# Kernel tuning notes

Hardware: AMD Instinct MI355X
Metric: run time of the kernel (lower is better)

The kernel has to match this reference:

```python
import jax, jax.numpy as jnp
import numpy as np

EMB = 256
N_NODES = 20000
N_EDGES = 200000


def _sage_layer(x, src, dst, edge_attr, W, b, n_nodes):
    # message = x[src] + edge_attr ; mean-aggregate into dst ; ReLU(Linear([x;agg]))
    msg = x[src] + edge_attr                                   # [2E, emb]
    s = jax.ops.segment_sum(msg, dst, num_segments=n_nodes)    # [N, emb]
    cnt = jax.ops.segment_sum(jnp.ones((dst.shape[0], 1), x.dtype), dst,
                              num_segments=n_nodes)            # [N, 1]
    agg = s / jnp.maximum(cnt, 1.0)
    return jax.nn.relu(jnp.concatenate([x, agg], axis=1) @ W + b)


def setup_inputs() -> dict:
    key = jax.random.key(0)
    ks = jax.random.split(key, 12)
    sc = 0.05
    inp = {
        "x": jax.random.normal(ks[0], (N_NODES, EMB), jnp.float32),
        "edge_attr": jax.random.normal(ks[1], (N_EDGES, EMB), jnp.float32),
        "batch_q_embds": jax.random.normal(ks[2], (N_EDGES, EMB), jnp.float32),
        "edge_index": jax.random.randint(ks[3], (2, N_EDGES), 0, N_NODES, jnp.int64
                                         if jax.config.jax_enable_x64 else jnp.int32),
        "W_rev1": jax.random.normal(ks[4], (EMB, EMB), jnp.float32) * sc,
        "b_rev1": jnp.zeros((EMB,), jnp.float32),
        "W_rev2": jax.random.normal(ks[5], (EMB, EMB), jnp.float32) * sc,
        "b_rev2": jnp.zeros((EMB,), jnp.float32),
        "W_sage1": jax.random.normal(ks[6], (2 * EMB, EMB), jnp.float32) * sc,
        "b_sage1": jnp.zeros((EMB,), jnp.float32),
        "W_sage2": jax.random.normal(ks[7], (2 * EMB, EMB), jnp.float32) * sc,
        "b_sage2": jnp.zeros((EMB,), jnp.float32),
        "W_pred1": jax.random.normal(ks[8], (6 * EMB, EMB), jnp.float32) * sc,
        "b_pred1": jnp.zeros((EMB,), jnp.float32),
        "W_pred2": jax.random.normal(ks[9], (EMB, 1), jnp.float32) * sc,
        "b_pred2": jnp.zeros((1,), jnp.float32),
    }
    return inp


def reference(x, edge_attr, batch_q_embds, edge_index,
              W_rev1, b_rev1, W_rev2, b_rev2,
              W_sage1, b_sage1, W_sage2, b_sage2,
              W_pred1, b_pred1, W_pred2, b_pred2):
    src, dst = edge_index[0], edge_index[1]
    # reverse-edge attributes via proj_reverse MLP
    edge_attr_rev = jax.nn.relu(edge_attr @ W_rev1 + b_rev1) @ W_rev2 + b_rev2
    src_f = jnp.concatenate([src, dst])          # [2E]
    dst_f = jnp.concatenate([dst, src])          # [2E]
    ea_f = jnp.concatenate([edge_attr, edge_attr_rev], axis=0)  # [2E, emb]
    # 2-layer GraphSAGE backbone over nodes, collect per-layer outputs
    h1 = _sage_layer(x, src_f, dst_f, ea_f, W_sage1, b_sage1, N_NODES)
    h2 = _sage_layer(h1, src_f, dst_f, ea_f, W_sage2, b_sage2, N_NODES)
    h_e = jnp.concatenate([h1, h2], axis=1)      # [N, 2*emb]
    # per-edge triple features: [q ; h_e[head] ; edge_attr ; h_e[tail]]
    h_triple = jnp.concatenate([batch_q_embds, h_e[src], edge_attr, h_e[dst]], axis=1)
    attn_logits = (jax.nn.relu(h_triple @ W_pred1 + b_pred1) @ W_pred2 + b_pred2)[:, 0]
    # idp-bern sampling (training=True): gumbel-like logistic noise, temp=1
    u = jax.random.uniform(jax.random.key(42), attn_logits.shape,
                           attn_logits.dtype, 1e-10, 1.0 - 1e-10)
    noise = jnp.log(u) - jnp.log(1.0 - u)
    sampled = jax.nn.sigmoid(attn_logits + noise)
    return attn_logits, sampled
```

## Files before the change

kernel.cpp:

```cpp
#include <hip/hip_runtime.h>
#include <cstdint>
#include <cstddef>

#define EMB 256
#define NN 20000
#define NE 200000
#define NE2 400000

typedef unsigned short ushort_t;
typedef __attribute__((ext_vector_type(8))) short bf16x8;
typedef __attribute__((ext_vector_type(4))) float f32x4;

__device__ __forceinline__ ushort_t f2bf(float f) {
    unsigned u = __float_as_uint(f);
    u += 0x7FFFu + ((u >> 16) & 1u);
    return (ushort_t)(u >> 16);
}
__device__ __forceinline__ float bf2f(ushort_t u) {
    return __uint_as_float(((unsigned)u) << 16);
}

__device__ __forceinline__ void async_cp16(const ushort_t* g, ushort_t* l) {
    __builtin_amdgcn_global_load_lds(
        (const __attribute__((address_space(1))) unsigned int*)g,
        (__attribute__((address_space(3))) unsigned int*)l,
        16, 0, 0);
}

__device__ __forceinline__ void pc_map(int bid, int T, int& p, int& colblk) {
    int Tf = T & ~15;
    if (bid < Tf) {
        p = (bid >> 4) * 8 + (bid & 7);
        colblk = (bid >> 3) & 1;
    } else {
        int rem = bid - Tf;
        int nr = (T - Tf) >> 1;
        p = (T >> 1) - nr + rem % nr;
        colblk = rem / nr;
    }
}

__device__ __forceinline__ unsigned rotl32(unsigned v, int d) {
    return (v << d) | (v >> (32 - d));
}
__device__ __forceinline__ void threefry2x32(unsigned k0, unsigned k1,
                                             unsigned x0, unsigned x1,
                                             unsigned& o0, unsigned& o1) {
    unsigned k2 = k0 ^ k1 ^ 0x1BD11BDAu;
    x0 += k0; x1 += k1;
#define TF_R(r) { x0 += x1; x1 = rotl32(x1, (r)); x1 ^= x0; }
    TF_R(13) TF_R(15) TF_R(26) TF_R(6)
    x0 += k1; x1 += k2 + 1u;
    TF_R(17) TF_R(29) TF_R(16) TF_R(24)
    x0 += k2; x1 += k0 + 2u;
    TF_R(13) TF_R(15) TF_R(26) TF_R(6)
    x0 += k0; x1 += k1 + 3u;
    TF_R(17) TF_R(29) TF_R(16) TF_R(24)
    x0 += k1; x1 += k2 + 4u;
    TF_R(13) TF_R(15) TF_R(26) TF_R(6)
    x0 += k2; x1 += k0 + 5u;
#undef TF_R
    o0 = x0; o1 = x1;
}

__global__ void deg_kernel(const int* __restrict__ src, const int* __restrict__ dst,
                           int* __restrict__ deg) {
    int i = blockIdx.x * blockDim.x + threadIdx.x;
    if (i < NE2) {
        int n = (i < NE) ? dst[i] : src[i - NE];
        atomicAdd(&deg[n], 1);
    }
}

__global__ void prefix_kernel(const int* __restrict__ deg, int* __restrict__ row_start,
                              int* __restrict__ cursor) {
    __shared__ int sums[1024];
    int t = threadIdx.x;
    const int CH = (NN + 1023) / 1024;
    int lo = t * CH, hi = lo + CH;
    if (hi > NN) hi = NN;
    if (lo > NN) lo = NN;
    int s = 0;
    for (int n = lo; n < hi; n++) s += deg[n];
    sums[t] = s;
    __syncthreads();
    for (int off = 1; off < 1024; off <<= 1) {
        int v = (t >= off) ? sums[t - off] : 0;
        __syncthreads();
        sums[t] += v;
        __syncthreads();
    }
    int run = (t == 0) ? 0 : sums[t - 1];
    for (int n = lo; n < hi; n++) {
        row_start[n] = run;
        cursor[n] = run;
        run += deg[n];
    }
    if (t == 1023) row_start[NN] = sums[1023];
}

__global__ void scatter_kernel(const int* __restrict__ src, const int* __restrict__ dst,
                               int* __restrict__ cursor, int* __restrict__ elist) {
    int i = blockIdx.x * blockDim.x + threadIdx.x;
    if (i < NE2) {
        int n = (i < NE) ? dst[i] : src[i - NE];
        int pos = atomicAdd(&cursor[n], 1);
        elist[pos] = i;
    }
}

__global__ void conv2_kernel(const float* __restrict__ a, ushort_t* __restrict__ oa, int na8,
                             const float* __restrict__ b, ushort_t* __restrict__ ob, int nb8) {
    int i = blockIdx.x * 256 + threadIdx.x;
    const float* p;
    ushort_t* o;
    if (i < na8) { p = a + (size_t)i * 8; o = oa + (size_t)i * 8; }
    else {
        int j = i - na8;
        if (j >= nb8) return;
        p = b + (size_t)j * 8; o = ob + (size_t)j * 8;
    }
    float4 u = *(const float4*)p;
    float4 v = *(const float4*)(p + 4);
    union { ushort_t s[8]; uint4 w; } r;
    r.s[0] = f2bf(u.x); r.s[1] = f2bf(u.y); r.s[2] = f2bf(u.z); r.s[3] = f2bf(u.w);
    r.s[4] = f2bf(v.x); r.s[5] = f2bf(v.y); r.s[6] = f2bf(v.z); r.s[7] = f2bf(v.w);
    *(uint4*)o = r.w;
}

struct TD { const float* src; ushort_t* dst; int stride, koff, kr; };
struct TA { TD d[8]; };

__global__ void transpose_all_kernel(TA ta) {
    TD t = ta.d[blockIdx.y];
    int k = blockIdx.x;
    if (k >= t.kr) return;
    int n = threadIdx.x;
    t.dst[(size_t)n * t.stride + t.koff + k] = f2bf(t.src[(size_t)k * 256 + n]);
}

__global__ __launch_bounds__(256, 3) void rev_fused_kernel(
        const ushort_t* __restrict__ ea_bf,
        const ushort_t* __restrict__ Wt1, const float* __restrict__ b1,
        const ushort_t* __restrict__ Wt2, const float* __restrict__ b2,
        ushort_t* __restrict__ ea_rev) {
    __shared__ ushort_t As[64 * 32];
    __shared__ ushort_t Bs[256 * 32];
    __shared__ ushort_t Hl[64 * 264];

    int tid = threadIdx.x;
    int lane = tid & 63, wave = tid >> 6;
    int wr = wave >> 1, wc = wave & 1;
    int quad = lane >> 4, col_l = lane & 15;
    int p = blockIdx.x;

    f32x4 acc[2][8];
#pragma unroll
    for (int mt = 0; mt < 2; mt++)
#pragma unroll
        for (int nt = 0; nt < 8; nt++) acc[mt][nt] = (f32x4)0.f;

    for (int k0 = 0; k0 < 256; k0 += 32) {
        __syncthreads();
        {
            int row = tid >> 2, ch = tid & 3;
            async_cp16(ea_bf + (size_t)(p * 64 + row) * 256 + k0 + ch * 8,
                       As + (wave * 64) * 8);
        }
#pragma unroll
        for (int j = 0; j < 4; j++) {
            int flat = tid + 256 * j;
            int n = flat >> 2, ch = flat & 3;
            async_cp16(Wt1 + (size_t)n * 256 + k0 + ch * 8,
                       Bs + (wave * 64 + 256 * j) * 8);
        }
        __syncthreads();
        bf16x8 a[2], b[8];
#pragma unroll
        for (int mt = 0; mt < 2; mt++)
            a[mt] = *(const bf16x8*)(As + (wr * 32 + mt * 16 + col_l) * 32 + quad * 8);
#pragma unroll
        for (int nt = 0; nt < 8; nt++)
            b[nt] = *(const bf16x8*)(Bs + (wc * 128 + nt * 16 + col_l) * 32 + quad * 8);
#pragma unroll
        for (int mt = 0; mt < 2; mt++)
#pragma unroll
            for (int nt = 0; nt < 8; nt++)
                acc[mt][nt] = __builtin_amdgcn_mfma_f32_16x16x32_bf16(
                    a[mt], b[nt], acc[mt][nt], 0, 0, 0);
    }

    __syncthreads();
#pragma unroll
    for (int nt = 0; nt < 8; nt++) {
        int lcol = wc * 128 + nt * 16 + col_l;
        float bb = b1[lcol];
#pragma unroll
        for (int mt = 0; mt < 2; mt++)
#pragma unroll
            for (int r = 0; r < 4; r++) {
                int lrow = wr * 32 + mt * 16 + quad * 4 + r;
                Hl[lrow * 264 + lcol] = f2bf(fmaxf(acc[mt][nt][r] + bb, 0.f));
            }
    }
#pragma unroll
    for (int mt = 0; mt < 2; mt++)
#pragma unroll
        for (int nt = 0; nt < 8; nt++) acc[mt][nt] = (f32x4)0.f;

    for (int k0 = 0; k0 < 256; k0 += 32) {
        __syncthreads();
#pragma unroll
        for (int j = 0; j < 4; j++) {
            int flat = tid + 256 * j;
            int n = flat >> 2, ch = flat & 3;
            async_cp16(Wt2 + (size_t)n * 256 + k0 + ch * 8,
                       Bs + (wave * 64 + 256 * j) * 8);
        }
        __syncthreads();
        bf16x8 a[2], b[8];
#pragma unroll
        for (int mt = 0; mt < 2; mt++)
            a[mt] = *(const bf16x8*)(Hl + (wr * 32 + mt * 16 + col_l) * 264
                                     + k0 + quad * 8);
#pragma unroll
        for (int nt = 0; nt < 8; nt++)
            b[nt] = *(const bf16x8*)(Bs + (wc * 128 + nt * 16 + col_l) * 32 + quad * 8);
#pragma unroll
        for (int mt = 0; mt < 2; mt++)
#pragma unroll
            for (int nt = 0; nt < 8; nt++)
                acc[mt][nt] = __builtin_amdgcn_mfma_f32_16x16x32_bf16(
                    a[mt], b[nt], acc[mt][nt], 0, 0, 0);
    }

#pragma unroll
    for (int nt = 0; nt < 8; nt++) {
        int colg = wc * 128 + nt * 16 + col_l;
        float bb = b2[colg];
#pragma unroll
        for (int mt = 0; mt < 2; mt++)
#pragma unroll
            for (int r = 0; r < 4; r++) {
                int rg = p * 64 + wr * 32 + mt * 16 + quad * 4 + r;
                ea_rev[(size_t)rg * 256 + colg] = f2bf(acc[mt][nt][r] + bb);
            }
    }
}

template <int KTOT, int EPI, bool A0F32>
__global__ __launch_bounds__(256, 4) void mfma_gemm(
        const void* __restrict__ A0v, int rsA0,
        const ushort_t* __restrict__ A1, int rsA1,
        const ushort_t* __restrict__ Bt, const ushort_t* __restrict__ Bt2,
        const float* __restrict__ bias,
        void* __restrict__ out, void* __restrict__ out2, int rsOut, int M,
        const int* __restrict__ srcp, const int* __restrict__ dstp,
        const float* __restrict__ Hs, const float* __restrict__ Hd,
        const float* __restrict__ w2) {
    __shared__ ushort_t As[2][128 * 32];
    __shared__ ushort_t Bs[2][128 * 32];
    __shared__ float red[128];

    int tid = threadIdx.x;
    int lane = tid & 63;
    int wave = tid >> 6;
    int wr = wave >> 1;
    int wc = wave & 1;
    int quad = lane >> 4;
    int col_l = lane & 15;
    int p, colblk;
    pc_map(blockIdx.x, gridDim.x, p, colblk);

    const ushort_t* Bsel = blockIdx.y ? Bt2 : Bt;
    void* Osel = blockIdx.y ? out2 : out;

    f32x4 acc[4][4];
#pragma unroll
    for (int mt = 0; mt < 4; mt++)
#pragma unroll
        for (int nt = 0; nt < 4; nt++) acc[mt][nt] = (f32x4)0.f;

    for (int k0 = 0; k0 < KTOT; k0 += 64) {
        __syncthreads();
#pragma unroll
        for (int h = 0; h < 2; h++) {
            int kk = k0 + 32 * h;
#pragma unroll
            for (int j = 0; j < 2; j++) {
                int flat = tid + 256 * j;
                int n = flat >> 2, ch = flat & 3;
                const ushort_t* gp = Bsel + (size_t)(colblk * 128 + n) * KTOT + kk + ch * 8;
                async_cp16(gp, Bs[h] + ((wave * 64 + 256 * j) * 8));
            }
            bool seg1 = (KTOT == 512) && (kk >= 256);
            if (A0F32 && !seg1) {
#pragma unroll
                for (int j = 0; j < 2; j++) {
                    int flat = tid + 256 * j;
                    int row = flat >> 2, ch = flat & 3;
                    int grow = p * 128 + row;
                    if (grow >= M) grow = M - 1;
                    const float* gp = (const float*)A0v + (size_t)grow * rsA0 + kk + ch * 8;
                    float4 u = *(const float4*)gp;
                    float4 v = *(const float4*)(gp + 4);
                    union { ushort_t s[8]; uint4 w; } r;
                    r.s[0] = f2bf(u.x); r.s[1] = f2bf(u.y); r.s[2] = f2bf(u.z); r.s[3] = f2bf(u.w);
                    r.s[4] = f2bf(v.x); r.s[5] = f2bf(v.y); r.s[6] = f2bf(v.z); r.s[7] = f2bf(v.w);
                    *(uint4*)(As[h] + (size_t)flat * 8) = r.w;
                }
            } else {
                const ushort_t* abase;
                int rs, koffs;
                if (KTOT == 512 && kk >= 256) { abase = A1; rs = rsA1; koffs = kk - 256; }
                else { abase = (const ushort_t*)A0v; rs = rsA0; koffs = kk; }
#pragma unroll
                for (int j = 0; j < 2; j++) {
                    int flat = tid + 256 * j;
                    int row = flat >> 2, ch = flat & 3;
                    int grow = p * 128 + row;
                    if (grow >= M) grow = M - 1;
                    const ushort_t* gp = abase + (size_t)grow * rs + koffs + ch * 8;
                    async_cp16(gp, As[h] + ((wave * 64 + 256 * j) * 8));
                }
            }
        }
        __syncthreads();

#pragma unroll
        for (int h = 0; h < 2; h++) {
            bf16x8 a[4], b[4];
#pragma unroll
            for (int mt = 0; mt < 4; mt++)
                a[mt] = *(const bf16x8*)(As[h] + (wr * 64 + mt * 16 + col_l) * 32 + quad * 8);
#pragma unroll
            for (int nt = 0; nt < 4; nt++)
                b[nt] = *(const bf16x8*)(Bs[h] + (wc * 64 + nt * 16 + col_l) * 32 + quad * 8);
#pragma unroll
            for (int mt = 0; mt < 4; mt++)
#pragma unroll
                for (int nt = 0; nt < 4; nt++)
                    acc[mt][nt] = __builtin_amdgcn_mfma_f32_16x16x32_bf16(
                        a[mt], b[nt], acc[mt][nt], 0, 0, 0);
        }
    }

    if (EPI == 4) {
        __syncthreads();
        if (tid < 128) red[tid] = 0.f;
        __syncthreads();
        float b1c[4], w2c[4];
#pragma unroll
        for (int nt = 0; nt < 4; nt++) {
            int col = colblk * 128 + wc * 64 + nt * 16 + col_l;
            b1c[nt] = bias[col];
            w2c[nt] = w2[col];
        }
#pragma unroll
        for (int mt = 0; mt < 4; mt++) {
#pragma unroll
            for (int r = 0; r < 4; r++) {
                int lrow = wr * 64 + mt * 16 + quad * 4 + r;
                int e = p * 128 + lrow;
                int ec = e < M ? e : M - 1;
                int s = srcp[ec], d = dstp[ec];
                const float* hsr = Hs + (size_t)s * 256;
                const float* hdr = Hd + (size_t)d * 256;
                float part = 0.f;
#pragma unroll
                for (int nt = 0; nt < 4; nt++) {
                    int col = colblk * 128 + wc * 64 + nt * 16 + col_l;
                    part += fmaxf(acc[mt][nt][r] + hsr[col] + hdr[col] + b1c[nt], 0.f)
                            * w2c[nt];
                }
#pragma unroll
                for (int m = 8; m > 0; m >>= 1) part += __shfl_xor(part, m, 64);
                if (col_l == 0) atomicAdd(&red[lrow], part);
            }
        }
        __syncthreads();
        if (tid < 128) {
            int e = p * 128 + tid;
            if (e < M) {
                float* tgt = colblk ? (float*)out2 : (float*)out;
                tgt[e] = red[tid];
            }
        }
        return;
    }

    float bs[4];
    if (EPI >= 2) {
#pragma unroll
        for (int nt = 0; nt < 4; nt++)
            bs[nt] = bias[colblk * 128 + wc * 64 + nt * 16 + col_l];
    }
#pragma unroll
    for (int mt = 0; mt < 4; mt++) {
#pragma unroll
        for (int nt = 0; nt < 4; nt++) {
            int colg = colblk * 128 + wc * 64 + nt * 16 + col_l;
#pragma unroll
            for (int r = 0; r < 4; r++) {
                int rg = p * 128 + wr * 64 + mt * 16 + quad * 4 + r;
                if (rg < M) {
                    float v = acc[mt][nt][r];
                    if (EPI >= 2) v += bs[nt];
                    if (EPI == 3) v = fmaxf(v, 0.f);
                    if (EPI == 0)
                        ((float*)Osel)[(size_t)rg * rsOut + colg] = v;
                    else
                        ((ushort_t*)Osel)[(size_t)rg * rsOut + colg] = f2bf(v);
                }
            }
        }
    }
}

__global__ void finalize_kernel(float* __restrict__ out, const float* __restrict__ part1,
                                const float* __restrict__ b2v, float* __restrict__ out_s) {
    int e = blockIdx.x * blockDim.x + threadIdx.x;
    if (e >= NE) return;
    float logit = out[e] + part1[e] + b2v[0];
    out[e] = logit;
    unsigned y0, y1;
    threefry2x32(0u, 42u, 0u, (unsigned)e, y0, y1);
    unsigned bits = y0 ^ y1;
    float f = __uint_as_float((bits >> 9) | 0x3F800000u) - 1.0f;
    float u = fmaxf(1e-10f, f + 1e-10f);
    float noise = logf(u) - logf(1.0f - u);
    out_s[e] = 1.0f / (1.0f + expf(-(logit + noise)));
}

__global__ __launch_bounds__(64) void agg_ea_kernel(
        const ushort_t* __restrict__ eaf, const ushort_t* __restrict__ ear,
        const int* __restrict__ row_start, const int* __restrict__ elist,
        float* __restrict__ agg_ea) {
    int n = blockIdx.x;
    int c = threadIdx.x * 4;
    float ax = 0.f, ay = 0.f, az = 0.f, aw = 0.f;
    int beg = row_start[n], end = row_start[n + 1];
    for (int p = beg; p < end; p++) {
        int i = elist[p];
        const ushort_t* er = (i < NE) ? eaf + (size_t)i * 256
                                      : ear + (size_t)(i - NE) * 256;
        ushort4 ev = *(const ushort4*)(er + c);
        ax += bf2f(ev.x); ay += bf2f(ev.y); az += bf2f(ev.z); aw += bf2f(ev.w);
    }
    float4 o; o.x = ax; o.y = ay; o.z = az; o.w = aw;
    *(float4*)(agg_ea + (size_t)n * 256 + c) = o;
}

__global__ __launch_bounds__(64) void agg_x_kernel(
        const ushort_t* __restrict__ xin, int rsx,
        const int* __restrict__ src, const int* __restrict__ dst,
        const int* __restrict__ row_start, const int* __restrict__ elist,
        const int* __restrict__ deg, const float* __restrict__ agg_ea,
        ushort_t* __restrict__ agg) {
    int n = blockIdx.x;
    int c = threadIdx.x * 4;
    float ax = 0.f, ay = 0.f, az = 0.f, aw = 0.f;
    int beg = row_start[n], end = row_start[n + 1];
    for (int p = beg; p < end; p++) {
        int i = elist[p];
        int node = (i < NE) ? src[i] : dst[i - NE];
        ushort4 xv = *(const ushort4*)(xin + (size_t)node * rsx + c);
        ax += bf2f(xv.x); ay += bf2f(xv.y); az += bf2f(xv.z); aw += bf2f(xv.w);
    }
    float4 e = *(const float4*)(agg_ea + (size_t)n * 256 + c);
    float d = fmaxf((float)deg[n], 1.0f);
    ushort4 o;
    o.x = f2bf((ax + e.x) / d); o.y = f2bf((ay + e.y) / d);
    o.z = f2bf((az + e.z) / d); o.w = f2bf((aw + e.w) / d);
    *(ushort4*)(agg + (size_t)n * 256 + c) = o;
}

extern "C" void kernel_launch(void* const* d_in, const int* in_sizes, int n_in,
                              void* d_out, int out_size, void* d_ws, size_t ws_size,
                              hipStream_t stream) {
    const float* x        = (const float*)d_in[0];
    const float* ea       = (const float*)d_in[1];
    const float* qemb     = (const float*)d_in[2];
    const int*   eidx     = (const int*)d_in[3];
    const float* W_rev1   = (const float*)d_in[4];
    const float* b_rev1   = (const float*)d_in[5];
    const float* W_rev2   = (const float*)d_in[6];
    const float* b_rev2   = (const float*)d_in[7];
    const float* W_sage1  = (const float*)d_in[8];
    const float* b_sage1  = (const float*)d_in[9];
    const float* W_sage2  = (const float*)d_in[10];
    const float* b_sage2  = (const float*)d_in[11];
    const float* W_pred1  = (const float*)d_in[12];
    const float* b_pred1  = (const float*)d_in[13];
    const float* W_pred2  = (const float*)d_in[14];
    const float* b_pred2  = (const float*)d_in[15];
    float* out = (float*)d_out;

    const int* src = eidx;
    const int* dst = eidx + NE;

    char* w = (char*)d_ws;
    ushort_t* ea_bf  = (ushort_t*)w; w += (size_t)NE * 256 * 2;
    ushort_t* ea_rev_bf = (ushort_t*)w; w += (size_t)NE * 256 * 2;
    ushort_t* x_bf   = (ushort_t*)w; w += (size_t)NN * 256 * 2;
    ushort_t* H      = (ushort_t*)w; w += (size_t)NN * 512 * 2;
    ushort_t* agg_bf = (ushort_t*)w; w += (size_t)NN * 256 * 2;
    float*    Hsrc   = (float*)w;    w += (size_t)NN * 256 * 4;
    float*    Hdst   = (float*)w;    w += (size_t)NN * 256 * 4;
    float*    part1  = (float*)w;    w += (size_t)NE * 4;
    ushort_t* Wt_rev1  = (ushort_t*)w; w += 256 * 256 * 2;
    ushort_t* Wt_rev2  = (ushort_t*)w; w += 256 * 256 * 2;
    ushort_t* Wt_sage1 = (ushort_t*)w; w += 256 * 512 * 2;
    ushort_t* Wt_sage2 = (ushort_t*)w; w += 256 * 512 * 2;
    ushort_t* Wt_src   = (ushort_t*)w; w += 256 * 512 * 2;
    ushort_t* Wt_dst   = (ushort_t*)w; w += 256 * 512 * 2;
    ushort_t* Wt_edge  = (ushort_t*)w; w += 256 * 512 * 2;
    int* deg       = (int*)w; w += (size_t)NN * 4;
    int* row_start = (int*)w; w += (size_t)(NN + 1) * 4;
    int* cursor    = (int*)w; w += (size_t)NN * 4;
    int* elist     = (int*)w; w += (size_t)NE2 * 4;

    float* agg_ea = Hsrc;

    const int EB = (NE + 127) / 128;
    const int NB = (NN + 127) / 128;

    hipMemsetAsync(deg, 0, (size_t)NN * 4, stream);
    deg_kernel<<<(NE2 + 255) / 256, 256, 0, stream>>>(src, dst, deg);
    prefix_kernel<<<1, 1024, 0, stream>>>(deg, row_start, cursor);
    scatter_kernel<<<(NE2 + 255) / 256, 256, 0, stream>>>(src, dst, cursor, elist);

    TA ta;
    ta.d[0] = { W_rev1,  Wt_rev1,  256, 0,   256 };
    ta.d[1] = { W_rev2,  Wt_rev2,  256, 0,   256 };
    ta.d[2] = { W_sage1, Wt_sage1, 512, 0,   512 };
    ta.d[3] = { W_sage2, Wt_sage2, 512, 0,   512 };
    ta.d[4] = { W_pred1 + (size_t)256 * 256,  Wt_src,  512, 0,   512 };
    ta.d[5] = { W_pred1 + (size_t)1024 * 256, Wt_dst,  512, 0,   512 };
    ta.d[6] = { W_pred1,                      Wt_edge, 512, 0,   256 };
    ta.d[7] = { W_pred1 + (size_t)768 * 256,  Wt_edge, 512, 256, 256 };
    transpose_all_kernel<<<dim3(512, 8), 256, 0, stream>>>(ta);

    conv2_kernel<<<((NE + NN) * 32 + 255) / 256, 256, 0, stream>>>(
        ea, ea_bf, NE * 32, x, x_bf, NN * 32);

    rev_fused_kernel<<<NE / 64, 256, 0, stream>>>(
        ea_bf, Wt_rev1, b_rev1, Wt_rev2, b_rev2, ea_rev_bf);

    agg_ea_kernel<<<NN, 64, 0, stream>>>(ea_bf, ea_rev_bf, row_start, elist, agg_ea);

    agg_x_kernel<<<NN, 64, 0, stream>>>(x_bf, 256, src, dst, row_start, elist,
                                        deg, agg_ea, agg_bf);
    mfma_gemm<512, 3, false><<<NB * 2, 256, 0, stream>>>(
        x_bf, 256, agg_bf, 256, Wt_sage1, nullptr, b_sage1,
        H, nullptr, 512, NN, nullptr, nullptr, nullptr, nullptr, nullptr);

    agg_x_kernel<<<NN, 64, 0, stream>>>(H, 512, src, dst, row_start, elist,
                                        deg, agg_ea, agg_bf);
    mfma_gemm<512, 3, false><<<NB * 2, 256, 0, stream>>>(
        H, 512, agg_bf, 256, Wt_sage2, nullptr, b_sage2,
        H + 256, nullptr, 512, NN, nullptr, nullptr, nullptr, nullptr, nullptr);

    mfma_gemm<512, 0, false><<<dim3(NB * 2, 2), 256, 0, stream>>>(
        H, 512, H + 256, 512, Wt_src, Wt_dst, nullptr,
        Hsrc, Hdst, 256, NN, nullptr, nullptr, nullptr, nullptr, nullptr);

    mfma_gemm<512, 4, true><<<EB * 2, 256, 0, stream>>>(
        qemb, 256, ea_bf, 256, Wt_edge, nullptr, b_pred1,
        out, part1, 0, NE, src, dst, Hsrc, Hdst, W_pred2);

    finalize_kernel<<<(NE + 255) / 256, 256, 0, stream>>>(out, part1, b_pred2, out + NE);
}
```

Measured before the change: 951.9 us.

## Pipeline GEMM main loop with register A operands and double-buffered LDS B

```diff
diff --git a/kernel.cpp b/kernel.cpp
--- a/kernel.cpp
+++ b/kernel.cpp
@@ -25,6 +25,10 @@
         (const __attribute__((address_space(1))) unsigned int*)g,
         (__attribute__((address_space(3))) unsigned int*)l,
         16, 0, 0);
+}
+
+__device__ __forceinline__ void waitbar4() {
+    asm volatile("s_waitcnt vmcnt(4) lgkmcnt(0)\n\ts_barrier" ::: "memory");
 }
 
 __device__ __forceinline__ void pc_map(int bid, int T, int& p, int& colblk) {
@@ -109,16 +113,20 @@
     }
 }
 
-__global__ void conv2_kernel(const float* __restrict__ a, ushort_t* __restrict__ oa, int na8,
-                             const float* __restrict__ b, ushort_t* __restrict__ ob, int nb8) {
+__global__ void conv3_kernel(const float* __restrict__ a, ushort_t* __restrict__ oa, int na8,
+                             const float* __restrict__ b, ushort_t* __restrict__ ob, int nb8,
+                             const float* __restrict__ c, ushort_t* __restrict__ oc, int nc8) {
     int i = blockIdx.x * 256 + threadIdx.x;
     const float* p;
     ushort_t* o;
     if (i < na8) { p = a + (size_t)i * 8; o = oa + (size_t)i * 8; }
-    else {
+    else if (i < na8 + nb8) {
         int j = i - na8;
-        if (j >= nb8) return;
         p = b + (size_t)j * 8; o = ob + (size_t)j * 8;
+    } else {
+        int j = i - na8 - nb8;
+        if (j >= nc8) return;
+        p = c + (size_t)j * 8; o = oc + (size_t)j * 8;
     }
     float4 u = *(const float4*)p;
     float4 v = *(const float4*)(p + 4);
@@ -248,9 +256,9 @@
     }
 }
 
-template <int KTOT, int EPI, bool A0F32>
-__global__ __launch_bounds__(256, 4) void mfma_gemm(
-        const void* __restrict__ A0v, int rsA0,
+template <int KTOT, int EPI>
+__global__ __launch_bounds__(256, 3) void mfma_gemm(
+        const ushort_t* __restrict__ A0, int rsA0,
         const ushort_t* __restrict__ A1, int rsA1,
         const ushort_t* __restrict__ Bt, const ushort_t* __restrict__ Bt2,
         const float* __restrict__ bias,
@@ -258,8 +266,8 @@
         const int* __restrict__ srcp, const int* __restrict__ dstp,
         const float* __restrict__ Hs, const float* __restrict__ Hd,
         const float* __restrict__ w2) {
-    __shared__ ushort_t As[2][128 * 32];
-    __shared__ ushort_t Bs[2][128 * 32];
+    __shared__ ushort_t Bs0[128 * 32];
+    __shared__ ushort_t Bs1[128 * 32];
     __shared__ float red[128];
 
     int tid = threadIdx.x;
@@ -281,68 +289,62 @@
 #pragma unroll
         for (int nt = 0; nt < 4; nt++) acc[mt][nt] = (f32x4)0.f;
 
-    for (int k0 = 0; k0 < KTOT; k0 += 64) {
-        __syncthreads();
-#pragma unroll
-        for (int h = 0; h < 2; h++) {
-            int kk = k0 + 32 * h;
-#pragma unroll
-            for (int j = 0; j < 2; j++) {
-                int flat = tid + 256 * j;
-                int n = flat >> 2, ch = flat & 3;
-                const ushort_t* gp = Bsel + (size_t)(colblk * 128 + n) * KTOT + kk + ch * 8;
-                async_cp16(gp, Bs[h] + ((wave * 64 + 256 * j) * 8));
-            }
-            bool seg1 = (KTOT == 512) && (kk >= 256);
-            if (A0F32 && !seg1) {
-#pragma unroll
-                for (int j = 0; j < 2; j++) {
-                    int flat = tid + 256 * j;
-                    int row = flat >> 2, ch = flat & 3;
-                    int grow = p * 128 + row;
-                    if (grow >= M) grow = M - 1;
-                    const float* gp = (const float*)A0v + (size_t)grow * rsA0 + kk + ch * 8;
-                    float4 u = *(const float4*)gp;
-                    float4 v = *(const float4*)(gp + 4);
-                    union { ushort_t s[8]; uint4 w; } r;
-                    r.s[0] = f2bf(u.x); r.s[1] = f2bf(u.y); r.s[2] = f2bf(u.z); r.s[3] = f2bf(u.w);
-                    r.s[4] = f2bf(v.x); r.s[5] = f2bf(v.y); r.s[6] = f2bf(v.z); r.s[7] = f2bf(v.w);
-                    *(uint4*)(As[h] + (size_t)flat * 8) = r.w;
-                }
-            } else {
-                const ushort_t* abase;
-                int rs, koffs;
-                if (KTOT == 512 && kk >= 256) { abase = A1; rs = rsA1; koffs = kk - 256; }
-                else { abase = (const ushort_t*)A0v; rs = rsA0; koffs = kk; }
-#pragma unroll
-                for (int j = 0; j < 2; j++) {
-                    int flat = tid + 256 * j;
-                    int row = flat >> 2, ch = flat & 3;
-                    int grow = p * 128 + row;
-                    if (grow >= M) grow = M - 1;
-                    const ushort_t* gp = abase + (size_t)grow * rs + koffs + ch * 8;
-                    async_cp16(gp, As[h] + ((wave * 64 + 256 * j) * 8));
-                }
-            }
-        }
-        __syncthreads();
-
-#pragma unroll
-        for (int h = 0; h < 2; h++) {
-            bf16x8 a[4], b[4];
-#pragma unroll
-            for (int mt = 0; mt < 4; mt++)
-                a[mt] = *(const bf16x8*)(As[h] + (wr * 64 + mt * 16 + col_l) * 32 + quad * 8);
+    const int NIT = KTOT / 32;
+
+    auto loadA = [&](bf16x8* a, int kt) {
+        int k0 = kt * 32;
+        const ushort_t* abase;
+        int rs, koffs;
+        if (KTOT == 512 && k0 >= 256) { abase = A1; rs = rsA1; koffs = k0 - 256; }
+        else                          { abase = A0; rs = rsA0; koffs = k0; }
+#pragma unroll
+        for (int mt = 0; mt < 4; mt++) {
+            int grow = p * 128 + wr * 64 + mt * 16 + col_l;
+            if (grow >= M) grow = M - 1;
+            a[mt] = *(const bf16x8*)(abase + (size_t)grow * rs + koffs + quad * 8);
+        }
+    };
+    auto stageB = [&](ushort_t* Bb, int kt) {
+        int k0 = kt * 32;
+#pragma unroll
+        for (int j = 0; j < 2; j++) {
+            int flat = tid + 256 * j;
+            int n = flat >> 2, ch = flat & 3;
+            async_cp16(Bsel + (size_t)(colblk * 128 + n) * KTOT + k0 + ch * 8,
+                       Bb + ((wave * 64 + 256 * j) * 8));
+        }
+    };
+    auto compute = [&](bf16x8* a, const ushort_t* Bb) {
+        bf16x8 b[4];
+#pragma unroll
+        for (int nt = 0; nt < 4; nt++)
+            b[nt] = *(const bf16x8*)(Bb + (wc * 64 + nt * 16 + col_l) * 32 + quad * 8);
+#pragma unroll
+        for (int mt = 0; mt < 4; mt++)
 #pragma unroll
             for (int nt = 0; nt < 4; nt++)
-                b[nt] = *(const bf16x8*)(Bs[h] + (wc * 64 + nt * 16 + col_l) * 32 + quad * 8);
-#pragma unroll
-            for (int mt = 0; mt < 4; mt++)
-#pragma unroll
-                for (int nt = 0; nt < 4; nt++)
-                    acc[mt][nt] = __builtin_amdgcn_mfma_f32_16x16x32_bf16(
-                        a[mt], b[nt], acc[mt][nt], 0, 0, 0);
-        }
+                acc[mt][nt] = __builtin_amdgcn_mfma_f32_16x16x32_bf16(
+                    a[mt], b[nt], acc[mt][nt], 0, 0, 0);
+    };
+
+    bf16x8 aA[4], aB[4];
+    loadA(aA, 0);
+    stageB(Bs0, 0);
+    loadA(aB, 1);
+    waitbar4();
+    stageB(Bs1, 1);
+
+    for (int k = 0; k < NIT; k += 2) {
+        int ke = (k + 2 < NIT) ? k + 2 : NIT - 1;
+        compute(aA, Bs0);
+        loadA(aA, ke);
+        waitbar4();
+        stageB(Bs0, ke);
+        int ko = (k + 3 < NIT) ? k + 3 : NIT - 1;
+        compute(aB, Bs1);
+        loadA(aB, ko);
+        waitbar4();
+        stageB(Bs1, ko);
     }
 
     if (EPI == 4) {
@@ -502,6 +504,7 @@
     char* w = (char*)d_ws;
     ushort_t* ea_bf  = (ushort_t*)w; w += (size_t)NE * 256 * 2;
     ushort_t* ea_rev_bf = (ushort_t*)w; w += (size_t)NE * 256 * 2;
+    ushort_t* q_bf   = (ushort_t*)w; w += (size_t)NE * 256 * 2;
     ushort_t* x_bf   = (ushort_t*)w; w += (size_t)NN * 256 * 2;
     ushort_t* H      = (ushort_t*)w; w += (size_t)NN * 512 * 2;
     ushort_t* agg_bf = (ushort_t*)w; w += (size_t)NN * 256 * 2;
@@ -541,8 +544,8 @@
     ta.d[7] = { W_pred1 + (size_t)768 * 256,  Wt_edge, 512, 256, 256 };
     transpose_all_kernel<<<dim3(512, 8), 256, 0, stream>>>(ta);
 
-    conv2_kernel<<<((NE + NN) * 32 + 255) / 256, 256, 0, stream>>>(
-        ea, ea_bf, NE * 32, x, x_bf, NN * 32);
+    conv3_kernel<<<((NE + NN + NE) * 32 + 255) / 256, 256, 0, stream>>>(
+        ea, ea_bf, NE * 32, x, x_bf, NN * 32, qemb, q_bf, NE * 32);
 
     rev_fused_kernel<<<NE / 64, 256, 0, stream>>>(
         ea_bf, Wt_rev1, b_rev1, Wt_rev2, b_rev2, ea_rev_bf);
@@ -551,22 +554,22 @@
 
     agg_x_kernel<<<NN, 64, 0, stream>>>(x_bf, 256, src, dst, row_start, elist,
                                         deg, agg_ea, agg_bf);
-    mfma_gemm<512, 3, false><<<NB * 2, 256, 0, stream>>>(
+    mfma_gemm<512, 3><<<NB * 2, 256, 0, stream>>>(
         x_bf, 256, agg_bf, 256, Wt_sage1, nullptr, b_sage1,
         H, nullptr, 512, NN, nullptr, nullptr, nullptr, nullptr, nullptr);
 
     agg_x_kernel<<<NN, 64, 0, stream>>>(H, 512, src, dst, row_start, elist,
                                         deg, agg_ea, agg_bf);
-    mfma_gemm<512, 3, false><<<NB * 2, 256, 0, stream>>>(
+    mfma_gemm<512, 3><<<NB * 2, 256, 0, stream>>>(
         H, 512, agg_bf, 256, Wt_sage2, nullptr, b_sage2,
         H + 256, nullptr, 512, NN, nullptr, nullptr, nullptr, nullptr, nullptr);
 
-    mfma_gemm<512, 0, false><<<dim3(NB * 2, 2), 256, 0, stream>>>(
+    mfma_gemm<512, 0><<<dim3(NB * 2, 2), 256, 0, stream>>>(
         H, 512, H + 256, 512, Wt_src, Wt_dst, nullptr,
         Hsrc, Hdst, 256, NN, nullptr, nullptr, nullptr, nullptr, nullptr);
 
-    mfma_gemm<512, 4, true><<<EB * 2, 256, 0, stream>>>(
-        qemb, 256, ea_bf, 256, Wt_edge, nullptr, b_pred1,
+    mfma_gemm<512, 4><<<EB * 2, 256, 0, stream>>>(
+        q_bf, 256, ea_bf, 256, Wt_edge, nullptr, b_pred1,
         out, part1, 0, NE, src, dst, Hsrc, Hdst, W_pred2);
 
     finalize_kernel<<<(NE + 255) / 256, 256, 0, stream>>>(out, part1, b_pred2, out + NE);
```

Measured after the change: 1.091 ms. +14.6%, slower.

## Read rev-MLP weights directly into registers and fuse first x/edge aggregation

Applied to the files above, without the earlier changes.

```diff
diff --git a/kernel.cpp b/kernel.cpp
--- a/kernel.cpp
+++ b/kernel.cpp
@@ -145,7 +145,6 @@
         const ushort_t* __restrict__ Wt2, const float* __restrict__ b2,
         ushort_t* __restrict__ ea_rev) {
     __shared__ ushort_t As[64 * 32];
-    __shared__ ushort_t Bs[256 * 32];
     __shared__ ushort_t Hl[64 * 264];
 
     int tid = threadIdx.x;
@@ -167,21 +166,16 @@
             async_cp16(ea_bf + (size_t)(p * 64 + row) * 256 + k0 + ch * 8,
                        As + (wave * 64) * 8);
         }
-#pragma unroll
-        for (int j = 0; j < 4; j++) {
-            int flat = tid + 256 * j;
-            int n = flat >> 2, ch = flat & 3;
-            async_cp16(Wt1 + (size_t)n * 256 + k0 + ch * 8,
-                       Bs + (wave * 64 + 256 * j) * 8);
-        }
-        __syncthreads();
-        bf16x8 a[2], b[8];
+        bf16x8 b[8];
+#pragma unroll
+        for (int nt = 0; nt < 8; nt++)
+            b[nt] = *(const bf16x8*)(Wt1 + (size_t)(wc * 128 + nt * 16 + col_l) * 256
+                                     + k0 + quad * 8);
+        __syncthreads();
+        bf16x8 a[2];
 #pragma unroll
         for (int mt = 0; mt < 2; mt++)
             a[mt] = *(const bf16x8*)(As + (wr * 32 + mt * 16 + col_l) * 32 + quad * 8);
-#pragma unroll
-        for (int nt = 0; nt < 8; nt++)
-            b[nt] = *(const bf16x8*)(Bs + (wc * 128 + nt * 16 + col_l) * 32 + quad * 8);
 #pragma unroll
         for (int mt = 0; mt < 2; mt++)
 #pragma unroll
@@ -190,7 +184,6 @@
                     a[mt], b[nt], acc[mt][nt], 0, 0, 0);
     }
 
-    __syncthreads();
 #pragma unroll
     for (int nt = 0; nt < 8; nt++) {
         int lcol = wc * 128 + nt * 16 + col_l;
@@ -207,25 +200,19 @@
     for (int mt = 0; mt < 2; mt++)
 #pragma unroll
         for (int nt = 0; nt < 8; nt++) acc[mt][nt] = (f32x4)0.f;
+    __syncthreads();
 
     for (int k0 = 0; k0 < 256; k0 += 32) {
-        __syncthreads();
-#pragma unroll
-        for (int j = 0; j < 4; j++) {
-            int flat = tid + 256 * j;
-            int n = flat >> 2, ch = flat & 3;
-            async_cp16(Wt2 + (size_t)n * 256 + k0 + ch * 8,
-                       Bs + (wave * 64 + 256 * j) * 8);
-        }
-        __syncthreads();
-        bf16x8 a[2], b[8];
+        bf16x8 b[8];
+#pragma unroll
+        for (int nt = 0; nt < 8; nt++)
+            b[nt] = *(const bf16x8*)(Wt2 + (size_t)(wc * 128 + nt * 16 + col_l) * 256
+                                     + k0 + quad * 8);
+        bf16x8 a[2];
 #pragma unroll
         for (int mt = 0; mt < 2; mt++)
             a[mt] = *(const bf16x8*)(Hl + (wr * 32 + mt * 16 + col_l) * 264
                                      + k0 + quad * 8);
-#pragma unroll
-        for (int nt = 0; nt < 8; nt++)
-            b[nt] = *(const bf16x8*)(Bs + (wc * 128 + nt * 16 + col_l) * 32 + quad * 8);
 #pragma unroll
         for (int mt = 0; mt < 2; mt++)
 #pragma unroll
@@ -432,23 +419,36 @@
     out_s[e] = 1.0f / (1.0f + expf(-(logit + noise)));
 }
 
-__global__ __launch_bounds__(64) void agg_ea_kernel(
+__global__ __launch_bounds__(64) void agg_xea_kernel(
+        const ushort_t* __restrict__ xin,
         const ushort_t* __restrict__ eaf, const ushort_t* __restrict__ ear,
+        const int* __restrict__ src, const int* __restrict__ dst,
         const int* __restrict__ row_start, const int* __restrict__ elist,
-        float* __restrict__ agg_ea) {
+        const int* __restrict__ deg, float* __restrict__ agg_ea,
+        ushort_t* __restrict__ agg) {
     int n = blockIdx.x;
     int c = threadIdx.x * 4;
-    float ax = 0.f, ay = 0.f, az = 0.f, aw = 0.f;
+    float sx0 = 0.f, sx1 = 0.f, sx2 = 0.f, sx3 = 0.f;
+    float se0 = 0.f, se1 = 0.f, se2 = 0.f, se3 = 0.f;
     int beg = row_start[n], end = row_start[n + 1];
     for (int p = beg; p < end; p++) {
         int i = elist[p];
-        const ushort_t* er = (i < NE) ? eaf + (size_t)i * 256
-                                      : ear + (size_t)(i - NE) * 256;
+        int node;
+        const ushort_t* er;
+        if (i < NE) { node = src[i]; er = eaf + (size_t)i * 256; }
+        else { int j = i - NE; node = dst[j]; er = ear + (size_t)j * 256; }
+        ushort4 xv = *(const ushort4*)(xin + (size_t)node * 256 + c);
         ushort4 ev = *(const ushort4*)(er + c);
-        ax += bf2f(ev.x); ay += bf2f(ev.y); az += bf2f(ev.z); aw += bf2f(ev.w);
-    }
-    float4 o; o.x = ax; o.y = ay; o.z = az; o.w = aw;
-    *(float4*)(agg_ea + (size_t)n * 256 + c) = o;
+        sx0 += bf2f(xv.x); sx1 += bf2f(xv.y); sx2 += bf2f(xv.z); sx3 += bf2f(xv.w);
+        se0 += bf2f(ev.x); se1 += bf2f(ev.y); se2 += bf2f(ev.z); se3 += bf2f(ev.w);
+    }
+    float4 eo; eo.x = se0; eo.y = se1; eo.z = se2; eo.w = se3;
+    *(float4*)(agg_ea + (size_t)n * 256 + c) = eo;
+    float d = fmaxf((float)deg[n], 1.0f);
+    ushort4 o;
+    o.x = f2bf((sx0 + se0) / d); o.y = f2bf((sx1 + se1) / d);
+    o.z = f2bf((sx2 + se2) / d); o.w = f2bf((sx3 + se3) / d);
+    *(ushort4*)(agg + (size_t)n * 256 + c) = o;
 }
 
 __global__ __launch_bounds__(64) void agg_x_kernel(
@@ -547,10 +547,9 @@
     rev_fused_kernel<<<NE / 64, 256, 0, stream>>>(
         ea_bf, Wt_rev1, b_rev1, Wt_rev2, b_rev2, ea_rev_bf);
 
-    agg_ea_kernel<<<NN, 64, 0, stream>>>(ea_bf, ea_rev_bf, row_start, elist, agg_ea);
-
-    agg_x_kernel<<<NN, 64, 0, stream>>>(x_bf, 256, src, dst, row_start, elist,
-                                        deg, agg_ea, agg_bf);
+    agg_xea_kernel<<<NN, 64, 0, stream>>>(x_bf, ea_bf, ea_rev_bf,
+                                          src, dst, row_start, elist, deg,
+                                          agg_ea, agg_bf);
     mfma_gemm<512, 3, false><<<NB * 2, 256, 0, stream>>>(
         x_bf, 256, agg_bf, 256, Wt_sage1, nullptr, b_sage1,
         H, nullptr, 512, NN, nullptr, nullptr, nullptr, nullptr, nullptr);
```

Result: slower. 1.021 ms (+7.3%).
